# Optimization experiments

Measured on AMD Instinct MI355X. Metric: run time of the kernel, lower is better.

Reference implementation:

```python
import jax, jax.numpy as jnp
import numpy as np

N = 32000   # nodes
E = 256000  # edges
G = 64      # graphs
IN = 64     # input feature dim
TD = 32     # time embedding dim
D = 128     # hidden dim
HEADS = 4
C = D // HEADS  # per-head channels = 32
ED = 16     # edge feature dim
L = 4       # num SBlocks
FF = 4 * D  # MLP hidden


def _ln(x, g, b):
    m = x.mean(-1, keepdims=True)
    v = ((x - m) ** 2).mean(-1, keepdims=True)
    return (x - m) / jnp.sqrt(v + 1e-5) * g + b


def _time_enc(t):
    half = TD // 2
    fac = jnp.exp(jnp.arange(half, dtype=jnp.float32) * (-jnp.log(10000.0) / (half - 1 + 1e-8)))
    ang = t.astype(jnp.float32)[:, None] * fac[None, :]
    return jnp.concatenate([jnp.sin(ang), jnp.cos(ang)], axis=-1)


def setup_inputs() -> dict:
    key = jax.random.key(0)
    ks = iter(jax.random.split(key, 64))
    nrm = lambda shape: jax.random.normal(next(ks), shape, dtype=jnp.float32) * 0.02
    x = jax.random.normal(next(ks), (N, IN), dtype=jnp.float32)
    t = jax.random.randint(next(ks), (N,), 0, 128, dtype=jnp.int32)
    edge_index = jax.random.randint(next(ks), (2, E), 0, N, dtype=jnp.int32)
    edge_attr = jax.random.normal(next(ks), (E, ED), dtype=jnp.float32)
    batch = jnp.sort(jax.random.randint(next(ks), (N,), 0, G, dtype=jnp.int32))
    p = {
        'Win': nrm((IN + TD, D)), 'b_in': jnp.zeros((D,), jnp.float32),
        'Wq': nrm((L, D, D)), 'bq': jnp.zeros((L, D), jnp.float32),
        'Wk': nrm((L, D, D)), 'bk': jnp.zeros((L, D), jnp.float32),
        'Wv': nrm((L, D, D)), 'bv': jnp.zeros((L, D), jnp.float32),
        'We': nrm((L, ED, D)), 'be': jnp.zeros((L, D), jnp.float32),
        'Wskip': nrm((L, D, D)), 'bskip': jnp.zeros((L, D), jnp.float32),
        'Wbeta': nrm((L, 3 * D)),
        'ln1_g': jnp.ones((L, D), jnp.float32), 'ln1_b': jnp.zeros((L, D), jnp.float32),
        'Wff1': nrm((L, D, FF)), 'bff1': jnp.zeros((L, FF), jnp.float32),
        'Wff2': nrm((L, FF, D)), 'bff2': jnp.zeros((L, D), jnp.float32),
        'ln2_g': jnp.ones((L, D), jnp.float32), 'ln2_b': jnp.zeros((L, D), jnp.float32),
        'Wh1': nrm((2 * D, D)), 'bh1': jnp.zeros((D,), jnp.float32),
        'Wh2': nrm((D, 2)), 'bh2': jnp.zeros((2,), jnp.float32),
    }
    return {'x': x, 't': t, 'edge_index': edge_index, 'edge_attr': edge_attr, 'batch': batch, **p}


def reference(x, t, edge_index, edge_attr, batch, Win, b_in, Wq, bq, Wk, bk, Wv, bv, We, be,
              Wskip, bskip, Wbeta, ln1_g, ln1_b, Wff1, bff1, Wff2, bff2, ln2_g, ln2_b,
              Wh1, bh1, Wh2, bh2):
    # input projection with sinusoidal time encoding
    h = jnp.concatenate([x, _time_enc(t)], axis=-1)
    h = jax.nn.relu(h @ Win + b_in)
    src, dst = edge_index[0], edge_index[1]
    for i in range(L):
        # TransformerConv (multi-head, edge_attr fused into key & value, beta skip)
        q = (h @ Wq[i] + bq[i]).reshape(N, HEADS, C)
        k = (h @ Wk[i] + bk[i]).reshape(N, HEADS, C)
        v = (h @ Wv[i] + bv[i]).reshape(N, HEADS, C)
        e = (edge_attr @ We[i] + be[i]).reshape(E, HEADS, C)
        kj = k[src] + e                     # [E,H,C] gather
        vj = v[src] + e
        alpha = (q[dst] * kj).sum(-1) / jnp.sqrt(jnp.asarray(C, h.dtype))  # [E,H]
        amax = jax.ops.segment_max(alpha, dst, num_segments=N)
        ex = jnp.exp(alpha - amax[dst])
        den = jax.ops.segment_sum(ex, dst, num_segments=N)
        w = ex / den[dst]                   # segment softmax over incoming edges
        out = jax.ops.segment_sum(vj * w[..., None], dst, num_segments=N).reshape(N, D)
        xr = h @ Wskip[i] + bskip[i]
        beta = jax.nn.sigmoid(jnp.concatenate([out, xr, out - xr], -1) @ Wbeta[i])[:, None]
        xs = beta * xr + (1.0 - beta) * out
        h = _ln(h + xs, ln1_g[i], ln1_b[i])
        ff = jax.nn.relu(h @ Wff1[i] + bff1[i]) @ Wff2[i] + bff2[i]
        h = _ln(h + ff, ln2_g[i], ln2_b[i])
    # last-timestep masked readout
    tf = t.astype(h.dtype)
    tmax = jax.ops.segment_max(tf, batch, num_segments=G)
    m = tf == tmax[batch]
    mf = m.astype(h.dtype)[:, None]
    cnt = jax.ops.segment_sum(mf, batch, num_segments=G)
    gmean = jax.ops.segment_sum(h * mf, batch, num_segments=G) / jnp.maximum(cnt, 1.0)
    gmax = jax.ops.segment_max(jnp.where(m[:, None], h, -1e30), batch, num_segments=G)
    g = jnp.concatenate([gmean, gmax], axis=-1)
    return jax.nn.relu(g @ Wh1 + bh1) @ Wh2 + bh2
```

## Files before the change

kernel.cpp:

```cpp
#include <hip/hip_runtime.h>

#define N_NODES 32000
#define N_EDGES 256000
#define N_GRAPH 64
#define NLAYER  4

typedef __attribute__((ext_vector_type(8))) short short8;
typedef __attribute__((ext_vector_type(4))) float f32x4;

__device__ __forceinline__ float bf2f(unsigned short u){
  return __uint_as_float(((unsigned int)u) << 16);
}
__device__ __forceinline__ unsigned short f2bf(float f){
  unsigned int x = __float_as_uint(f);
  x = x + 0x7fffu + ((x >> 16) & 1u);
  return (unsigned short)(x >> 16);
}
__device__ __forceinline__ float ldf(const void* p, int i, int isbf){
  if(isbf) return bf2f(((const unsigned short*)p)[i]);
  return ((const float*)p)[i];
}

__global__ void TactileGAT_43207370997900_kernel() {}

__global__ void sentinel_kernel(unsigned short* out){
  int i = blockIdx.x * 64 + threadIdx.x;
  if(i < 2 * N_GRAPH) out[i] = (unsigned short)0x4000;
}

__global__ void detect_kernel(const unsigned int* ones_words, int* flag){
  if(blockIdx.x == 0 && threadIdx.x == 0)
    flag[0] = (ones_words[0] == 0x3F800000u) ? 0 : 1;
}

__global__ void zero_kernel(int* p, int n){
  int i = blockIdx.x * 256 + threadIdx.x;
  if(i < n) p[i] = 0;
}

__global__ void deg_kernel(const int* dst, int* deg){
  int e = blockIdx.x * 256 + threadIdx.x;
  if(e < N_EDGES) atomicAdd(&deg[dst[e]], 1);
}

__global__ void blocksum_kernel(const int* deg, int* psum){
  __shared__ int s[256];
  int b = blockIdx.x, tid = threadIdx.x;
  int i = b * 256 + tid;
  s[tid] = (i < N_NODES) ? deg[i] : 0;
  __syncthreads();
  for(int off = 128; off > 0; off = off / 2){
    if(tid < off) s[tid] = s[tid] + s[tid + off];
    __syncthreads();
  }
  if(tid == 0) psum[b] = s[0];
}

__global__ void scanp_kernel(int* psum){
  __shared__ int s[128];
  int tid = threadIdx.x;
  int v = (tid < 125) ? psum[tid] : 0;
  s[tid] = v;
  __syncthreads();
  for(int off = 1; off < 128; off = off * 2){
    int tv = (tid >= off) ? s[tid - off] : 0;
    __syncthreads();
    s[tid] = s[tid] + tv;
    __syncthreads();
  }
  if(tid < 125) psum[tid] = s[tid] - v;
}

__global__ void rowptr_kernel(const int* deg, const int* psum, int* rowptr,
                              int* cursor){
  __shared__ int s[256];
  int b = blockIdx.x, tid = threadIdx.x;
  int i = b * 256 + tid;
  int v = (i < N_NODES) ? deg[i] : 0;
  s[tid] = v;
  __syncthreads();
  for(int off = 1; off < 256; off = off * 2){
    int tv = (tid >= off) ? s[tid - off] : 0;
    __syncthreads();
    s[tid] = s[tid] + tv;
    __syncthreads();
  }
  int excl = s[tid] - v + psum[b];
  if(i < N_NODES){ rowptr[i] = excl; cursor[i] = excl; }
  if(i == N_NODES - 1) rowptr[N_NODES] = excl + v;
}

__global__ void scatter_kernel(const int* dst, int* cursor, int* csr){
  int e = blockIdx.x * 256 + threadIdx.x;
  if(e < N_EDGES){
    int pos = atomicAdd(&cursor[dst[e]], 1);
    csr[pos] = e;
  }
}

__global__ void pack_kernel(const void* Wq, const void* Wk, const void* Wv,
                            const void* Wsk, const void* Wff1, const void* Wff2,
                            const int* flag, unsigned short* WTq,
                            unsigned short* WT1, unsigned short* WT2){
  int idx = blockIdx.x * 256 + threadIdx.x;
  int isbf = flag[0];
  int i = idx / 196608;
  if(i >= NLAYER) return;
  int rem = idx - i * 196608;
  int seg = rem / 65536;
  int off = rem - seg * 65536;
  if(seg == 0){
    int n = off >> 7, k = off & 127;
    int sel = n >> 7, c = n & 127;
    const void* W = (sel == 0) ? Wq : (sel == 1) ? Wk : (sel == 2) ? Wv : Wsk;
    WTq[i * 65536 + off] = f2bf(ldf(W, i * 16384 + k * 128 + c, isbf));
  } else if(seg == 1){
    int n = off >> 7, k = off & 127;
    WT1[i * 65536 + off] = f2bf(ldf(Wff1, i * 65536 + k * 512 + n, isbf));
  } else {
    int n = off >> 9, k = off & 511;
    WT2[i * 65536 + off] = f2bf(ldf(Wff2, i * 65536 + k * 128 + n, isbf));
  }
}

__global__ void input_proj_kernel(const void* x, const int* t, const void* Win,
                                  const void* b_in, const int* flag,
                                  unsigned short* h){
  __shared__ float in_s[96];
  int n = blockIdx.x, d = threadIdx.x;
  int isbf = flag[0];
  if(d < 64){
    in_s[d] = ldf(x, n * 64 + d, isbf);
  } else if(d < 96){
    int j  = d - 64;
    int jj = (j < 16) ? j : (j - 16);
    float fac = expf((float)jj * (-9.210340371976184f / 15.00000001f));
    float ang = (float)t[n] * fac;
    in_s[d] = (j < 16) ? sinf(ang) : cosf(ang);
  }
  __syncthreads();
  float acc = ldf(b_in, d, isbf);
  for(int k = 0; k < 96; k++) acc += in_s[k] * ldf(Win, k * 128 + d, isbf);
  h[n * 128 + d] = f2bf(fmaxf(acc, 0.f));
}

__global__ void gemm_frag(const unsigned short* A, const unsigned short* WT,
                          const void* bias, int boff, const int* flag,
                          int K, int nbx, void* Y, int obf, int ystride,
                          int act){
  int tid = threadIdx.x;
  int bx = blockIdx.x % nbx;
  int by = blockIdx.x / nbx;
  int m0 = by * 128, c0 = bx * 128;
  int wv = tid / 64, lane = tid % 64;
  int q = lane / 16, r = lane % 16;
  const unsigned short* Ap0 = A + (m0 + wv * 32 + r) * K + q * 8;
  const unsigned short* Ap1 = Ap0 + 16 * K;
  const unsigned short* Wp = WT + (c0 + r) * K + q * 8;
  f32x4 acc[2][8];
  for(int g = 0; g < 2; g++)
    for(int tt = 0; tt < 8; tt++)
      for(int i = 0; i < 4; i++) acc[g][tt][i] = 0.f;
  for(int k0 = 0; k0 < K; k0 += 32){
    short8 a0 = *(const short8*)(Ap0 + k0);
    short8 a1 = *(const short8*)(Ap1 + k0);
    for(int tt = 0; tt < 8; tt++){
      short8 b8 = *(const short8*)(Wp + tt * 16 * K + k0);
      acc[0][tt] = __builtin_amdgcn_mfma_f32_16x16x32_bf16(a0, b8, acc[0][tt], 0, 0, 0);
      acc[1][tt] = __builtin_amdgcn_mfma_f32_16x16x32_bf16(a1, b8, acc[1][tt], 0, 0, 0);
    }
  }
  int isbf = flag[0];
  for(int tt = 0; tt < 8; tt++){
    int c = c0 + tt * 16 + r;
    float bv = ldf(bias, boff + c, isbf);
    for(int g = 0; g < 2; g++){
      for(int i = 0; i < 4; i++){
        int row = m0 + wv * 32 + g * 16 + q * 4 + i;
        float v = acc[g][tt][i] + bv;
        if(act == 1) v = fmaxf(v, 0.f);
        if(obf) ((unsigned short*)Y)[row * ystride + c] = f2bf(v);
        else    ((float*)Y)[row * ystride + c] = v;
      }
    }
  }
}

__global__ void qkvs_frag(const unsigned short* A, const unsigned short* WTq,
                          const void* b0, const void* b1, const void* b2,
                          const void* b3, int boff, const int* flag,
                          float* qs, unsigned int* kvp){
  int tid = threadIdx.x;
  int sel = blockIdx.x % 4;
  int by  = blockIdx.x / 4;
  int m0 = by * 128;
  int wv = tid / 64, lane = tid % 64;
  int q = lane / 16, r = lane % 16;
  const unsigned short* Ap0 = A + (m0 + wv * 32 + r) * 128 + q * 8;
  const unsigned short* Ap1 = Ap0 + 16 * 128;
  const unsigned short* Wp = WTq + (sel * 128 + r) * 128 + q * 8;
  f32x4 acc[2][8];
  for(int g = 0; g < 2; g++)
    for(int tt = 0; tt < 8; tt++)
      for(int i = 0; i < 4; i++) acc[g][tt][i] = 0.f;
  for(int k0 = 0; k0 < 128; k0 += 32){
    short8 a0 = *(const short8*)(Ap0 + k0);
    short8 a1 = *(const short8*)(Ap1 + k0);
    for(int tt = 0; tt < 8; tt++){
      short8 b8 = *(const short8*)(Wp + tt * 16 * 128 + k0);
      acc[0][tt] = __builtin_amdgcn_mfma_f32_16x16x32_bf16(a0, b8, acc[0][tt], 0, 0, 0);
      acc[1][tt] = __builtin_amdgcn_mfma_f32_16x16x32_bf16(a1, b8, acc[1][tt], 0, 0, 0);
    }
  }
  int isbf = flag[0];
  const void* B = (sel == 0) ? b0 : (sel == 1) ? b1 : (sel == 2) ? b2 : b3;
  if(sel == 0 || sel == 3){
    for(int tt = 0; tt < 8; tt++){
      int cc = tt * 16 + r;
      float bv = ldf(B, boff + cc, isbf);
      for(int g = 0; g < 2; g++){
        for(int i = 0; i < 4; i++){
          int row = m0 + wv * 32 + g * 16 + q * 4 + i;
          float v = acc[g][tt][i] + bv;
          if(sel == 0) qs[row * 256 + cc] = v;
          else         qs[row * 256 + 128 + cc] = v;
        }
      }
    }
  } else {
    int base = (sel - 1) * 64;
    for(int tt = 0; tt < 4; tt++){
      int cc0 = tt * 16 + r;
      float bv0 = ldf(B, boff + cc0, isbf);
      float bv1 = ldf(B, boff + cc0 + 64, isbf);
      for(int g = 0; g < 2; g++){
        for(int i = 0; i < 4; i++){
          int row = m0 + wv * 32 + g * 16 + q * 4 + i;
          unsigned int w = (unsigned int)f2bf(acc[g][tt][i] + bv0)
                         | ((unsigned int)f2bf(acc[g][tt + 4][i] + bv1) << 16);
          kvp[row * 128 + base + cc0] = w;
        }
      }
    }
  }
}

#define CH 4
__global__ void attn_epi1_kernel(const float* qs, const unsigned int* kvp,
                                 const void* edge_attr, const int* esrc,
                                 const int* rowptr, const int* csr,
                                 const void* We, int weoff, const void* be, int beoff,
                                 const void* Wbeta, int wboff,
                                 const void* lng, int lgoff,
                                 const void* lnb, int lboff,
                                 const unsigned short* h, const int* flag,
                                 unsigned short* h2){
  __shared__ float sea[CH * 16];
  __shared__ float sprod[CH * 144];
  __shared__ float svj[CH * 128];
  __shared__ float salpha[CH * 4];
  __shared__ float red[64];
  int n = blockIdx.x, L = threadIdx.x;
  int isbf = flag[0];
  int hL = L >> 5, c = L & 31;
  float q0 = qs[n * 256 + L]      * 0.17677669529663687f;
  float q1 = qs[n * 256 + 64 + L] * 0.17677669529663687f;
  float wec0[16], wec1[16];
  for(int j = 0; j < 16; j++){
    wec0[j] = ldf(We, weoff + j * 128 + L, isbf);
    wec1[j] = ldf(We, weoff + j * 128 + 64 + L, isbf);
  }
  float be0 = ldf(be, beoff + L, isbf);
  float be1 = ldf(be, beoff + 64 + L, isbf);
  float m0 = -1e30f, l0 = 0.f, acc0 = 0.f;
  float m1 = -1e30f, l1 = 0.f, acc1 = 0.f;
  int beg = rowptr[n], end = rowptr[n + 1];
  for(int ci = beg; ci < end; ci += CH){
    int Ep = end - ci; if(Ep > CH) Ep = CH;
    for(int tt = L; tt < Ep * 16; tt += 64){
      int i = tt >> 4, j = tt & 15;
      sea[tt] = ldf(edge_attr, csr[ci + i] * 16 + j, isbf);
    }
    unsigned int kws[CH], vws[CH];
    for(int i = 0; i < CH; i++){
      if(i < Ep){
        int src = esrc[csr[ci + i]];
        kws[i] = kvp[src * 128 + L];
        vws[i] = kvp[src * 128 + 64 + L];
      }
    }
    __syncthreads();
    for(int i = 0; i < Ep; i++){
      const f32x4* sp = (const f32x4*)(sea + i * 16);
      f32x4 e0 = sp[0], e1 = sp[1], e2 = sp[2], e3 = sp[3];
      float ea[16];
      *(f32x4*)(ea + 0)  = e0; *(f32x4*)(ea + 4)  = e1;
      *(f32x4*)(ea + 8)  = e2; *(f32x4*)(ea + 12) = e3;
      float ed0 = be0, ed1 = be1;
      for(int j = 0; j < 16; j++){
        ed0 += ea[j] * wec0[j];
        ed1 += ea[j] * wec1[j];
      }
      float kd0 = bf2f((unsigned short)(kws[i] & 0xffffu)) + ed0;
      float kd1 = bf2f((unsigned short)(kws[i] >> 16)) + ed1;
      float vd0 = bf2f((unsigned short)(vws[i] & 0xffffu)) + ed0;
      float vd1 = bf2f((unsigned short)(vws[i] >> 16)) + ed1;
      sprod[i * 144 + hL * 36 + c]       = q0 * kd0;
      sprod[i * 144 + (2 + hL) * 36 + c] = q1 * kd1;
      svj[i * 128 + L]      = vd0;
      svj[i * 128 + 64 + L] = vd1;
    }
    __syncthreads();
    if(L < 16){
      int i = L >> 2, h4 = L & 3;
      if(i < Ep){
        const f32x4* pp = (const f32x4*)(sprod + i * 144 + h4 * 36);
        float s = 0.f;
        for(int tq = 0; tq < 8; tq++){
          f32x4 v4 = pp[tq];
          s += v4[0] + v4[1] + v4[2] + v4[3];
        }
        salpha[i * 4 + h4] = s;
      }
    }
    __syncthreads();
    float mc0 = -1e30f, mc1 = -1e30f;
    for(int i = 0; i < Ep; i++){
      float a0 = salpha[i * 4 + hL];
      float a1 = salpha[i * 4 + 2 + hL];
      mc0 = fmaxf(mc0, a0);
      mc1 = fmaxf(mc1, a1);
    }
    float mn0 = fmaxf(m0, mc0);
    float mn1 = fmaxf(m1, mc1);
    float sc0 = expf(m0 - mn0);
    float sc1 = expf(m1 - mn1);
    l0 = l0 * sc0; acc0 = acc0 * sc0;
    l1 = l1 * sc1; acc1 = acc1 * sc1;
    for(int i = 0; i < Ep; i++){
      float p0 = expf(salpha[i * 4 + hL] - mn0);
      float p1 = expf(salpha[i * 4 + 2 + hL] - mn1);
      l0 += p0; acc0 += p0 * svj[i * 128 + L];
      l1 += p1; acc1 += p1 * svj[i * 128 + 64 + L];
    }
    m0 = mn0; m1 = mn1;
    __syncthreads();
  }
  float o0 = (l0 > 0.f) ? acc0 / l0 : 0.f;
  float o1 = (l1 > 0.f) ? acc1 / l1 : 0.f;
  float xr0 = qs[n * 256 + 128 + L];
  float xr1 = qs[n * 256 + 192 + L];
  float hv0 = bf2f(h[n * 128 + L]);
  float hv1 = bf2f(h[n * 128 + 64 + L]);
  float part = o0 * ldf(Wbeta, wboff + L, isbf)
             + xr0 * ldf(Wbeta, wboff + 128 + L, isbf)
             + (o0 - xr0) * ldf(Wbeta, wboff + 256 + L, isbf)
             + o1 * ldf(Wbeta, wboff + 64 + L, isbf)
             + xr1 * ldf(Wbeta, wboff + 192 + L, isbf)
             + (o1 - xr1) * ldf(Wbeta, wboff + 320 + L, isbf);
  red[L] = part;
  __syncthreads();
  for(int off = 32; off > 0; off = off / 2){
    if(L < off) red[L] = red[L] + red[L + off];
    __syncthreads();
  }
  float beta = 1.f / (1.f + expf(-red[0]));
  __syncthreads();
  float y0 = hv0 + beta * xr0 + (1.f - beta) * o0;
  float y1 = hv1 + beta * xr1 + (1.f - beta) * o1;
  red[L] = y0 + y1;
  __syncthreads();
  for(int off = 32; off > 0; off = off / 2){
    if(L < off) red[L] = red[L] + red[L + off];
    __syncthreads();
  }
  float mean = red[0] * (1.f / 128.f);
  __syncthreads();
  float dy0 = y0 - mean, dy1 = y1 - mean;
  red[L] = dy0 * dy0 + dy1 * dy1;
  __syncthreads();
  for(int off = 32; off > 0; off = off / 2){
    if(L < off) red[L] = red[L] + red[L + off];
    __syncthreads();
  }
  float var = red[0] * (1.f / 128.f);
  float inv = 1.f / sqrtf(var + 1e-5f);
  h2[n * 128 + L]      = f2bf(dy0 * inv * ldf(lng, lgoff + L, isbf)
                              + ldf(lnb, lboff + L, isbf));
  h2[n * 128 + 64 + L] = f2bf(dy1 * inv * ldf(lng, lgoff + 64 + L, isbf)
                              + ldf(lnb, lboff + 64 + L, isbf));
}

__global__ void ff2_ln_kernel(const unsigned short* A, const unsigned short* WT,
                              const void* bias, int boff,
                              const unsigned short* h2,
                              const void* lng, int lgoff,
                              const void* lnb, int lboff,
                              const int* flag, unsigned short* outh){
  __shared__ float Ys[64 * 133];
  __shared__ float smean[64];
  __shared__ float sinv[64];
  int tid = threadIdx.x;
  int m0 = blockIdx.x * 64;
  int wv = tid / 64, lane = tid % 64;
  int q = lane / 16, r = lane % 16;
  const unsigned short* Ap = A + (m0 + wv * 16 + r) * 512 + q * 8;
  const unsigned short* Wp = WT + r * 512 + q * 8;
  f32x4 acc[8];
  for(int tt = 0; tt < 8; tt++)
    for(int i = 0; i < 4; i++) acc[tt][i] = 0.f;
  for(int k0 = 0; k0 < 512; k0 += 32){
    short8 a8 = *(const short8*)(Ap + k0);
    for(int tt = 0; tt < 8; tt++){
      short8 b8 = *(const short8*)(Wp + tt * 16 * 512 + k0);
      acc[tt] = __builtin_amdgcn_mfma_f32_16x16x32_bf16(a8, b8, acc[tt], 0, 0, 0);
    }
  }
  int isbf = flag[0];
  for(int tt = 0; tt < 8; tt++){
    int c = tt * 16 + r;
    float bv = ldf(bias, boff + c, isbf);
    for(int i = 0; i < 4; i++){
      int rl = wv * 16 + q * 4 + i;
      float v = acc[tt][i] + bv;
      Ys[rl * 133 + c] = bf2f(h2[(m0 + rl) * 128 + c]) + v;
    }
  }
  __syncthreads();
  if(tid < 64){
    float s = 0.f, s2 = 0.f;
    for(int c = 0; c < 128; c++){
      float y = Ys[tid * 133 + c];
      s += y; s2 += y * y;
    }
    float mean = s * (1.f / 128.f);
    float var  = s2 * (1.f / 128.f) - mean * mean;
    smean[tid] = mean;
    sinv[tid]  = 1.f / sqrtf(var + 1e-5f);
  }
  __syncthreads();
  for(int tt = 0; tt < 8; tt++){
    int c = tt * 16 + r;
    float g = ldf(lng, lgoff + c, isbf);
    float b = ldf(lnb, lboff + c, isbf);
    for(int i = 0; i < 4; i++){
      int rl = wv * 16 + q * 4 + i;
      float y = Ys[rl * 133 + c];
      outh[(m0 + rl) * 128 + c] = f2bf((y - smean[rl]) * sinv[rl] * g + b);
    }
  }
}

__global__ void bounds_kernel(const int* batch, int* gstart, int* gend){
  int n = blockIdx.x * 256 + threadIdx.x;
  if(n >= N_NODES) return;
  int b = batch[n];
  if(n == 0 || batch[n - 1] != b) gstart[b] = n;
  if(n == N_NODES - 1 || batch[n + 1] != b) gend[b] = n + 1;
}

__global__ void readout_kernel(const int* t, const unsigned short* h,
                               const int* gstart, const int* gend, float* gbuf){
  __shared__ int redi[128];
  int g = blockIdx.x, d = threadIdx.x;
  int s = gstart[g], e = gend[g];
  int tm = -2147483647;
  for(int nn = s + d; nn < e; nn += 128){
    int tv = t[nn];
    tm = (tv > tm) ? tv : tm;
  }
  redi[d] = tm;
  __syncthreads();
  for(int off = 64; off > 0; off = off / 2){
    if(d < off) redi[d] = (redi[d + off] > redi[d]) ? redi[d + off] : redi[d];
    __syncthreads();
  }
  tm = redi[0];
  float sum = 0.f, mx = -1e30f;
  int cnt = 0;
  for(int nn = s; nn < e; nn++){
    if(t[nn] == tm){
      float hv = bf2f(h[nn * 128 + d]);
      sum += hv;
      mx = fmaxf(mx, hv);
      cnt = cnt + 1;
    }
  }
  gbuf[g * 256 + d]       = sum / (float)((cnt < 1) ? 1 : cnt);
  gbuf[g * 256 + 128 + d] = mx;
}

__global__ void mlp_kernel(const float* gbuf, const void* Wh1, const void* bh1,
                           const void* Wh2, const void* bh2, const int* flag,
                           void* outp){
  __shared__ float gs[256];
  __shared__ float r1[128];
  int g = blockIdx.x, d = threadIdx.x;
  int isbf = flag[0];
  gs[d]       = gbuf[g * 256 + d];
  gs[d + 128] = gbuf[g * 256 + 128 + d];
  __syncthreads();
  float acc = ldf(bh1, d, isbf);
  for(int k = 0; k < 256; k++) acc += gs[k] * ldf(Wh1, k * 128 + d, isbf);
  r1[d] = fmaxf(acc, 0.f);
  __syncthreads();
  if(d < 2){
    float a = ldf(bh2, d, isbf);
    for(int k = 0; k < 128; k++) a += r1[k] * ldf(Wh2, k * 2 + d, isbf);
    if(isbf) ((unsigned short*)outp)[g * 2 + d] = f2bf(a);
    else     ((float*)outp)[g * 2 + d] = a;
  }
}

extern "C" void kernel_launch(void* const* d_in, const int* in_sizes, int n_in,
                              void* d_out, int out_size, void* d_ws, size_t ws_size,
                              hipStream_t stream){
  const void* x          = d_in[0];
  const int*  t          = (const int*)d_in[1];
  const int*  edge_index = (const int*)d_in[2];
  const void* edge_attr  = d_in[3];
  const int*  batch      = (const int*)d_in[4];
  const void* Win  = d_in[5];  const void* b_in = d_in[6];
  const void* Wq   = d_in[7];  const void* bq   = d_in[8];
  const void* Wk   = d_in[9];  const void* bk   = d_in[10];
  const void* Wv   = d_in[11]; const void* bv   = d_in[12];
  const void* We   = d_in[13]; const void* be   = d_in[14];
  const void* Wsk  = d_in[15]; const void* bsk  = d_in[16];
  const void* Wbeta= d_in[17];
  const void* ln1g = d_in[18]; const void* ln1b = d_in[19];
  const void* Wff1 = d_in[20]; const void* bff1 = d_in[21];
  const void* Wff2 = d_in[22]; const void* bff2 = d_in[23];
  const void* ln2g = d_in[24]; const void* ln2b = d_in[25];
  const void* Wh1  = d_in[26]; const void* bh1  = d_in[27];
  const void* Wh2  = d_in[28]; const void* bh2  = d_in[29];
  (void)in_sizes; (void)n_in; (void)out_size; (void)ws_size;

  char* p = (char*)d_ws;
  unsigned short* h    = (unsigned short*)p; p += (long long)N_NODES * 128 * 2;
  unsigned short* h2   = (unsigned short*)p; p += (long long)N_NODES * 128 * 2;
  float* qs            = (float*)p;          p += (long long)N_NODES * 256 * 4;
  unsigned int* kvp    = (unsigned int*)p;   p += (long long)N_NODES * 128 * 4;
  unsigned short* ffmid= (unsigned short*)p; p += (long long)N_NODES * 512 * 2;
  unsigned short* WTq  = (unsigned short*)p; p += (long long)NLAYER * 65536 * 2;
  unsigned short* WT1  = (unsigned short*)p; p += (long long)NLAYER * 65536 * 2;
  unsigned short* WT2  = (unsigned short*)p; p += (long long)NLAYER * 65536 * 2;
  float* gbuf = (float*)p; p += (long long)N_GRAPH * 256 * 4;
  int* flag   = (int*)p;   p += 4;
  int* rowptr = (int*)p;   p += (long long)(N_NODES + 1) * 4;
  int* cursor = (int*)p;   p += (long long)N_NODES * 4;
  int* deg    = (int*)p;   p += (long long)N_NODES * 4;
  int* gstart = (int*)p;   p += (long long)N_GRAPH * 4;
  int* gend   = (int*)p;   p += (long long)N_GRAPH * 4;
  int* psum   = (int*)p;   p += 128 * 4;
  int* csr    = (int*)p;   p += (long long)N_EDGES * 4;

  const int* esrc = edge_index;
  const int* edst = edge_index + N_EDGES;

  sentinel_kernel<<<2, 64, 0, stream>>>((unsigned short*)d_out);
  detect_kernel<<<1, 64, 0, stream>>>((const unsigned int*)ln1g, flag);

  int n_zero = N_NODES + 2 * N_GRAPH;
  zero_kernel<<<(n_zero + 255) / 256, 256, 0, stream>>>(deg, n_zero);

  pack_kernel<<<(NLAYER * 196608 + 255) / 256, 256, 0, stream>>>(
      Wq, Wk, Wv, Wsk, Wff1, Wff2, flag, WTq, WT1, WT2);
  deg_kernel<<<N_EDGES / 256, 256, 0, stream>>>(edst, deg);
  blocksum_kernel<<<125, 256, 0, stream>>>(deg, psum);
  scanp_kernel<<<1, 128, 0, stream>>>(psum);
  rowptr_kernel<<<125, 256, 0, stream>>>(deg, psum, rowptr, cursor);
  scatter_kernel<<<N_EDGES / 256, 256, 0, stream>>>(edst, cursor, csr);
  input_proj_kernel<<<N_NODES, 128, 0, stream>>>(x, t, Win, b_in, flag, h);

  int nby = N_NODES / 128;
  for(int i = 0; i < NLAYER; i++){
    qkvs_frag<<<4 * nby, 256, 0, stream>>>(
        h, WTq + (long long)i * 65536, bq, bk, bv, bsk, i * 128, flag, qs, kvp);
    attn_epi1_kernel<<<N_NODES, 64, 0, stream>>>(
        qs, kvp, edge_attr, esrc, rowptr, csr, We, i * 2048, be, i * 128,
        Wbeta, i * 384, ln1g, i * 128, ln1b, i * 128, h, flag, h2);
    gemm_frag<<<4 * nby, 256, 0, stream>>>(
        h2, WT1 + (long long)i * 65536, bff1, i * 512, flag, 128, 4,
        ffmid, 1, 512, 1);
    ff2_ln_kernel<<<N_NODES / 64, 256, 0, stream>>>(
        ffmid, WT2 + (long long)i * 65536, bff2, i * 128, h2,
        ln2g, i * 128, ln2b, i * 128, flag, h);
  }

  bounds_kernel<<<N_NODES / 256, 256, 0, stream>>>(batch, gstart, gend);
  readout_kernel<<<N_GRAPH, 128, 0, stream>>>(t, h, gstart, gend, gbuf);
  mlp_kernel<<<N_GRAPH, 128, 0, stream>>>(gbuf, Wh1, bh1, Wh2, bh2, flag, d_out);
}
```

Baseline: 1.058 ms.

## Rewrite edge attention as one-wave-per-node streaming softmax with prefetch

The attention kernel now runs one 64-lane wave per node, four nodes per block, and processes incoming edges one at a time with an online softmax. The next edge's key/value and edge attributes are prefetched a step ahead, and head dot products and LayerNorm reductions use cross-lane shuffles instead of shared memory and barriers. CSR entries now store (edge, src) pairs, edge attributes are pre-converted to fp32, and K/V are interleaved so one uint2 load fetches both. This targets the many __syncthreads and the dependent index loads of the chunked version, at the cost of extra workspace and an edge-attribute conversion pass, which is repeated every layer if workspace is short.

```diff
diff --git a/kernel.cpp b/kernel.cpp
--- a/kernel.cpp
+++ b/kernel.cpp
@@ -90,12 +90,18 @@
   if(i == N_NODES - 1) rowptr[N_NODES] = excl + v;
 }
 
-__global__ void scatter_kernel(const int* dst, int* cursor, int* csr){
+__global__ void scatter_kernel(const int* dst, const int* src, int* cursor,
+                               int2* csr2){
   int e = blockIdx.x * 256 + threadIdx.x;
   if(e < N_EDGES){
     int pos = atomicAdd(&cursor[dst[e]], 1);
-    csr[pos] = e;
-  }
+    csr2[pos] = make_int2(e, src[e]);
+  }
+}
+
+__global__ void ea32_kernel(const void* ea, const int* flag, float* eaf){
+  int i = blockIdx.x * 256 + threadIdx.x;
+  if(i < N_EDGES * 16) eaf[i] = ldf(ea, i, flag[0]);
 }
 
 __global__ void pack_kernel(const void* Wq, const void* Wk, const void* Wv,
@@ -228,7 +234,7 @@
       }
     }
   } else {
-    int base = (sel - 1) * 64;
+    int voff = sel - 1;
     for(int tt = 0; tt < 4; tt++){
       int cc0 = tt * 16 + r;
       float bv0 = ldf(B, boff + cc0, isbf);
@@ -238,116 +244,98 @@
           int row = m0 + wv * 32 + g * 16 + q * 4 + i;
           unsigned int w = (unsigned int)f2bf(acc[g][tt][i] + bv0)
                          | ((unsigned int)f2bf(acc[g][tt + 4][i] + bv1) << 16);
-          kvp[row * 128 + base + cc0] = w;
+          kvp[row * 128 + 2 * cc0 + voff] = w;
         }
       }
     }
   }
 }
 
-#define CH 4
-__global__ void attn_epi1_kernel(const float* qs, const unsigned int* kvp,
-                                 const void* edge_attr, const int* esrc,
-                                 const int* rowptr, const int* csr,
-                                 const void* We, int weoff, const void* be, int beoff,
-                                 const void* Wbeta, int wboff,
-                                 const void* lng, int lgoff,
-                                 const void* lnb, int lboff,
-                                 const unsigned short* h, const int* flag,
-                                 unsigned short* h2){
-  __shared__ float sea[CH * 16];
-  __shared__ float sprod[CH * 144];
-  __shared__ float svj[CH * 128];
-  __shared__ float salpha[CH * 4];
-  __shared__ float red[64];
-  int n = blockIdx.x, L = threadIdx.x;
-  int isbf = flag[0];
-  int hL = L >> 5, c = L & 31;
-  float q0 = qs[n * 256 + L]      * 0.17677669529663687f;
-  float q1 = qs[n * 256 + 64 + L] * 0.17677669529663687f;
+#define ATTN_WPB 4
+__global__ __launch_bounds__(256, 4)
+void attn_epi1_kernel(const float* __restrict__ qs,
+                      const unsigned int* __restrict__ kvp,
+                      const float* __restrict__ eaf,
+                      const int2* __restrict__ csr2,
+                      const int* __restrict__ rowptr,
+                      const void* __restrict__ We, int weoff,
+                      const void* __restrict__ be, int beoff,
+                      const void* __restrict__ Wbeta, int wboff,
+                      const void* __restrict__ lng, int lgoff,
+                      const void* __restrict__ lnb, int lboff,
+                      const unsigned short* __restrict__ h,
+                      const int* __restrict__ flag,
+                      unsigned short* __restrict__ h2){
+  int wv = threadIdx.x >> 6, L = threadIdx.x & 63;
+  int n = blockIdx.x * ATTN_WPB + wv;
+  int isbf = flag[0];
   float wec0[16], wec1[16];
+#pragma unroll
   for(int j = 0; j < 16; j++){
     wec0[j] = ldf(We, weoff + j * 128 + L, isbf);
     wec1[j] = ldf(We, weoff + j * 128 + 64 + L, isbf);
   }
   float be0 = ldf(be, beoff + L, isbf);
   float be1 = ldf(be, beoff + 64 + L, isbf);
-  float m0 = -1e30f, l0 = 0.f, acc0 = 0.f;
-  float m1 = -1e30f, l1 = 0.f, acc1 = 0.f;
+  float q0 = qs[n * 256 + L]      * 0.17677669529663687f;
+  float q1 = qs[n * 256 + 64 + L] * 0.17677669529663687f;
   int beg = rowptr[n], end = rowptr[n + 1];
-  for(int ci = beg; ci < end; ci += CH){
-    int Ep = end - ci; if(Ep > CH) Ep = CH;
-    for(int tt = L; tt < Ep * 16; tt += 64){
-      int i = tt >> 4, j = tt & 15;
-      sea[tt] = ldf(edge_attr, csr[ci + i] * 16 + j, isbf);
-    }
-    unsigned int kws[CH], vws[CH];
-    for(int i = 0; i < CH; i++){
-      if(i < Ep){
-        int src = esrc[csr[ci + i]];
-        kws[i] = kvp[src * 128 + L];
-        vws[i] = kvp[src * 128 + 64 + L];
-      }
-    }
-    __syncthreads();
-    for(int i = 0; i < Ep; i++){
-      const f32x4* sp = (const f32x4*)(sea + i * 16);
-      f32x4 e0 = sp[0], e1 = sp[1], e2 = sp[2], e3 = sp[3];
-      float ea[16];
-      *(f32x4*)(ea + 0)  = e0; *(f32x4*)(ea + 4)  = e1;
-      *(f32x4*)(ea + 8)  = e2; *(f32x4*)(ea + 12) = e3;
-      float ed0 = be0, ed1 = be1;
-      for(int j = 0; j < 16; j++){
-        ed0 += ea[j] * wec0[j];
-        ed1 += ea[j] * wec1[j];
-      }
-      float kd0 = bf2f((unsigned short)(kws[i] & 0xffffu)) + ed0;
-      float kd1 = bf2f((unsigned short)(kws[i] >> 16)) + ed1;
-      float vd0 = bf2f((unsigned short)(vws[i] & 0xffffu)) + ed0;
-      float vd1 = bf2f((unsigned short)(vws[i] >> 16)) + ed1;
-      sprod[i * 144 + hL * 36 + c]       = q0 * kd0;
-      sprod[i * 144 + (2 + hL) * 36 + c] = q1 * kd1;
-      svj[i * 128 + L]      = vd0;
-      svj[i * 128 + 64 + L] = vd1;
-    }
-    __syncthreads();
-    if(L < 16){
-      int i = L >> 2, h4 = L & 3;
-      if(i < Ep){
-        const f32x4* pp = (const f32x4*)(sprod + i * 144 + h4 * 36);
-        float s = 0.f;
-        for(int tq = 0; tq < 8; tq++){
-          f32x4 v4 = pp[tq];
-          s += v4[0] + v4[1] + v4[2] + v4[3];
-        }
-        salpha[i * 4 + h4] = s;
-      }
-    }
-    __syncthreads();
-    float mc0 = -1e30f, mc1 = -1e30f;
-    for(int i = 0; i < Ep; i++){
-      float a0 = salpha[i * 4 + hL];
-      float a1 = salpha[i * 4 + 2 + hL];
-      mc0 = fmaxf(mc0, a0);
-      mc1 = fmaxf(mc1, a1);
-    }
-    float mn0 = fmaxf(m0, mc0);
-    float mn1 = fmaxf(m1, mc1);
-    float sc0 = expf(m0 - mn0);
-    float sc1 = expf(m1 - mn1);
-    l0 = l0 * sc0; acc0 = acc0 * sc0;
-    l1 = l1 * sc1; acc1 = acc1 * sc1;
-    for(int i = 0; i < Ep; i++){
-      float p0 = expf(salpha[i * 4 + hL] - mn0);
-      float p1 = expf(salpha[i * 4 + 2 + hL] - mn1);
-      l0 += p0; acc0 += p0 * svj[i * 128 + L];
-      l1 += p1; acc1 += p1 * svj[i * 128 + 64 + L];
-    }
-    m0 = mn0; m1 = mn1;
-    __syncthreads();
-  }
-  float o0 = (l0 > 0.f) ? acc0 / l0 : 0.f;
-  float o1 = (l1 > 0.f) ? acc1 / l1 : 0.f;
+  float m0 = -1e30f, l0 = 0.f, a0s = 0.f;
+  float m1 = -1e30f, l1 = 0.f, a1s = 0.f;
+  uint2 kvN = make_uint2(0u, 0u);
+  f32x4 eN0 = 0.f, eN1 = 0.f, eN2 = 0.f, eN3 = 0.f;
+  int2 esB = make_int2(0, 0);
+  if(beg < end){
+    int2 esA = csr2[beg];
+    int e = __builtin_amdgcn_readfirstlane(esA.x);
+    int s = __builtin_amdgcn_readfirstlane(esA.y);
+    kvN = *(const uint2*)(kvp + (size_t)s * 128 + 2 * L);
+    const f32x4* ep = (const f32x4*)(eaf + (size_t)e * 16);
+    eN0 = ep[0]; eN1 = ep[1]; eN2 = ep[2]; eN3 = ep[3];
+    if(beg + 1 < end) esB = csr2[beg + 1];
+  }
+  for(int ci = beg; ci < end; ci++){
+    uint2 kv = kvN;
+    f32x4 E0 = eN0, E1 = eN1, E2 = eN2, E3 = eN3;
+    int2 esC = esB;
+    if(ci + 2 < end) esC = csr2[ci + 2];
+    if(ci + 1 < end){
+      int e = __builtin_amdgcn_readfirstlane(esB.x);
+      int s = __builtin_amdgcn_readfirstlane(esB.y);
+      kvN = *(const uint2*)(kvp + (size_t)s * 128 + 2 * L);
+      const f32x4* ep = (const f32x4*)(eaf + (size_t)e * 16);
+      eN0 = ep[0]; eN1 = ep[1]; eN2 = ep[2]; eN3 = ep[3];
+      esB = esC;
+    }
+    float ea[16];
+    *(f32x4*)(ea + 0)  = E0; *(f32x4*)(ea + 4)  = E1;
+    *(f32x4*)(ea + 8)  = E2; *(f32x4*)(ea + 12) = E3;
+    float ed0 = be0, ed1 = be1;
+#pragma unroll
+    for(int j = 0; j < 16; j++){
+      ed0 += ea[j] * wec0[j];
+      ed1 += ea[j] * wec1[j];
+    }
+    float kd0 = bf2f((unsigned short)(kv.x & 0xffffu)) + ed0;
+    float kd1 = bf2f((unsigned short)(kv.x >> 16)) + ed1;
+    float vd0 = bf2f((unsigned short)(kv.y & 0xffffu)) + ed0;
+    float vd1 = bf2f((unsigned short)(kv.y >> 16)) + ed1;
+    float p0 = q0 * kd0, p1 = q1 * kd1;
+#pragma unroll
+    for(int mk = 1; mk < 32; mk <<= 1){
+      p0 += __shfl_xor(p0, mk, 64);
+      p1 += __shfl_xor(p1, mk, 64);
+    }
+    float mn0 = fmaxf(m0, p0), mn1 = fmaxf(m1, p1);
+    float g0 = __expf(fminf(p0, m0) - mn0);
+    float g1 = __expf(fminf(p1, m1) - mn1);
+    float pp0 = (p0 <= m0) ? g0 : 1.f, sc0 = (p0 <= m0) ? 1.f : g0;
+    float pp1 = (p1 <= m1) ? g1 : 1.f, sc1 = (p1 <= m1) ? 1.f : g1;
+    l0 = l0 * sc0 + pp0;  a0s = a0s * sc0 + pp0 * vd0;  m0 = mn0;
+    l1 = l1 * sc1 + pp1;  a1s = a1s * sc1 + pp1 * vd1;  m1 = mn1;
+  }
+  float o0 = (l0 > 0.f) ? a0s / l0 : 0.f;
+  float o1 = (l1 > 0.f) ? a1s / l1 : 0.f;
   float xr0 = qs[n * 256 + 128 + L];
   float xr1 = qs[n * 256 + 192 + L];
   float hv0 = bf2f(h[n * 128 + L]);
@@ -358,33 +346,20 @@
              + o1 * ldf(Wbeta, wboff + 64 + L, isbf)
              + xr1 * ldf(Wbeta, wboff + 192 + L, isbf)
              + (o1 - xr1) * ldf(Wbeta, wboff + 320 + L, isbf);
-  red[L] = part;
-  __syncthreads();
-  for(int off = 32; off > 0; off = off / 2){
-    if(L < off) red[L] = red[L] + red[L + off];
-    __syncthreads();
-  }
-  float beta = 1.f / (1.f + expf(-red[0]));
-  __syncthreads();
+#pragma unroll
+  for(int mk = 1; mk < 64; mk <<= 1) part += __shfl_xor(part, mk, 64);
+  float beta = 1.f / (1.f + __expf(-part));
   float y0 = hv0 + beta * xr0 + (1.f - beta) * o0;
   float y1 = hv1 + beta * xr1 + (1.f - beta) * o1;
-  red[L] = y0 + y1;
-  __syncthreads();
-  for(int off = 32; off > 0; off = off / 2){
-    if(L < off) red[L] = red[L] + red[L + off];
-    __syncthreads();
-  }
-  float mean = red[0] * (1.f / 128.f);
-  __syncthreads();
+  float s = y0 + y1;
+#pragma unroll
+  for(int mk = 1; mk < 64; mk <<= 1) s += __shfl_xor(s, mk, 64);
+  float mean = s * (1.f / 128.f);
   float dy0 = y0 - mean, dy1 = y1 - mean;
-  red[L] = dy0 * dy0 + dy1 * dy1;
-  __syncthreads();
-  for(int off = 32; off > 0; off = off / 2){
-    if(L < off) red[L] = red[L] + red[L + off];
-    __syncthreads();
-  }
-  float var = red[0] * (1.f / 128.f);
-  float inv = 1.f / sqrtf(var + 1e-5f);
+  float v2 = dy0 * dy0 + dy1 * dy1;
+#pragma unroll
+  for(int mk = 1; mk < 64; mk <<= 1) v2 += __shfl_xor(v2, mk, 64);
+  float inv = 1.f / sqrtf(v2 * (1.f / 128.f) + 1e-5f);
   h2[n * 128 + L]      = f2bf(dy0 * inv * ldf(lng, lgoff + L, isbf)
                               + ldf(lnb, lboff + L, isbf));
   h2[n * 128 + 64 + L] = f2bf(dy1 * inv * ldf(lng, lgoff + 64 + L, isbf)
@@ -533,7 +508,7 @@
   const void* ln2g = d_in[24]; const void* ln2b = d_in[25];
   const void* Wh1  = d_in[26]; const void* bh1  = d_in[27];
   const void* Wh2  = d_in[28]; const void* bh2  = d_in[29];
-  (void)in_sizes; (void)n_in; (void)out_size; (void)ws_size;
+  (void)in_sizes; (void)n_in; (void)out_size;
 
   char* p = (char*)d_ws;
   unsigned short* h    = (unsigned short*)p; p += (long long)N_NODES * 128 * 2;
@@ -552,7 +527,17 @@
   int* gstart = (int*)p;   p += (long long)N_GRAPH * 4;
   int* gend   = (int*)p;   p += (long long)N_GRAPH * 4;
   int* psum   = (int*)p;   p += 128 * 4;
-  int* csr    = (int*)p;   p += (long long)N_EDGES * 4;
+  int2* csr2  = (int2*)p;  p += (long long)N_EDGES * 8;
+
+  size_t base_used = (size_t)(p - (char*)d_ws);
+  size_t eaf_bytes = (size_t)N_EDGES * 16 * 4;
+  float* eaf;
+  int ea_dedicated;
+  if(ws_size >= base_used + eaf_bytes){
+    eaf = (float*)p; ea_dedicated = 1;
+  } else {
+    eaf = (float*)ffmid; ea_dedicated = 0;
+  }
 
   const int* esrc = edge_index;
   const int* edst = edge_index + N_EDGES;
@@ -569,15 +554,19 @@
   blocksum_kernel<<<125, 256, 0, stream>>>(deg, psum);
   scanp_kernel<<<1, 128, 0, stream>>>(psum);
   rowptr_kernel<<<125, 256, 0, stream>>>(deg, psum, rowptr, cursor);
-  scatter_kernel<<<N_EDGES / 256, 256, 0, stream>>>(edst, cursor, csr);
+  scatter_kernel<<<N_EDGES / 256, 256, 0, stream>>>(edst, esrc, cursor, csr2);
   input_proj_kernel<<<N_NODES, 128, 0, stream>>>(x, t, Win, b_in, flag, h);
+  if(ea_dedicated)
+    ea32_kernel<<<(N_EDGES * 16) / 256, 256, 0, stream>>>(edge_attr, flag, eaf);
 
   int nby = N_NODES / 128;
   for(int i = 0; i < NLAYER; i++){
+    if(!ea_dedicated)
+      ea32_kernel<<<(N_EDGES * 16) / 256, 256, 0, stream>>>(edge_attr, flag, eaf);
     qkvs_frag<<<4 * nby, 256, 0, stream>>>(
         h, WTq + (long long)i * 65536, bq, bk, bv, bsk, i * 128, flag, qs, kvp);
-    attn_epi1_kernel<<<N_NODES, 64, 0, stream>>>(
-        qs, kvp, edge_attr, esrc, rowptr, csr, We, i * 2048, be, i * 128,
+    attn_epi1_kernel<<<N_NODES / ATTN_WPB, 256, 0, stream>>>(
+        qs, kvp, eaf, csr2, rowptr, We, i * 2048, be, i * 128,
         Wbeta, i * 384, ln1g, i * 128, ln1b, i * 128, h, flag, h2);
     gemm_frag<<<4 * nby, 256, 0, stream>>>(
         h2, WT1 + (long long)i * 65536, bff1, i * 512, flag, 128, 4,
```

Result: slower. 1.128 ms (+6.6%).
